# Kernel optimization log

Hardware: AMD Instinct MI355X
Metric: run time of the kernel (lower is better)

## Reference

```python
import jax, jax.numpy as jnp
import numpy as np

VOCAB = 50257
NSAMPLES = 1048576


def setup_inputs() -> dict:
    key = jax.random.key(0)
    k1, k2 = jax.random.split(key)
    # positive sampling weights (need not be normalized, as in WeightedRandomSampler)
    frequencies = jax.random.uniform(k1, (VOCAB,), dtype=jnp.float32) + 1e-3
    # pre-drawn uniforms, one per sample (replacement=True => iid draws)
    u = jax.random.uniform(k2, (NSAMPLES,), dtype=jnp.float32)
    return {"frequencies": frequencies, "u": u}


def reference(frequencies, u):
    # WeightedRandomSampler with replacement == multinomial sampling proportional
    # to frequencies. Implemented as inverse-CDF: normalize, cumsum, binary search.
    cdf = jnp.cumsum(frequencies)          # [V], unnormalized CDF
    total = cdf[-1]
    # scale uniforms into [0, total) instead of dividing the whole CDF (fewer ops)
    idx = jnp.searchsorted(cdf, u * total, side="right")  # [N] int indices
    idx = jnp.clip(idx, 0, frequencies.shape[0] - 1)
    # original returns a FloatTensor of the sampled indices
    return idx.astype(jnp.float32)
```

## Files before the change

kernel.cpp:

```cpp
#include <hip/hip_runtime.h>
#include <math.h>


#define GRP 4
#define TPB 512
#define SPT 4

__device__ __forceinline__ int physIdx(int i) { return i + (i >> 5); }

__global__ __launch_bounds__(256) void gsum_kernel(const float* __restrict__ freq,
                                                   int V, float* __restrict__ gsum) {
    const int g = blockIdx.x * 256 + threadIdx.x;
    const int G = (V + 3) >> 2;
    if (g >= G) return;
    const int base = g * 4;
    float s = 0.f;
    if (base + 3 < V) {
        const float4 v = *reinterpret_cast<const float4*>(freq + base);
        s = v.x + v.y + v.z + v.w;
    } else {
        for (int j = 0; j < 4; ++j)
            if (base + j < V) s += freq[base + j];
    }
    gsum[g] = s;
}

template <int PAD>
__global__ __launch_bounds__(TPB) void sample_kernel(const float* __restrict__ freq,
                                                     const float* __restrict__ u,
                                                     const float* __restrict__ gsum,
                                                     float* __restrict__ out,
                                                     int N, int V, int G) {
    constexpr int GPTM = PAD / TPB;
    __shared__ float sS[PAD + (PAD >> 5)];
    __shared__ float wsum[TPB / 64];
    const int t = threadIdx.x;
    const int lane = t & 63;
    const int w = t >> 6;
    const int GPT = (G + TPB - 1) / TPB;

    const int gid = blockIdx.x * TPB + t;
    const long long i0 = (long long)gid * SPT;
    float uk[SPT];
    const bool full = (i0 + SPT <= N);
    if (full) {
        const float4 A = *reinterpret_cast<const float4*>(u + i0);
        uk[0] = A.x; uk[1] = A.y; uk[2] = A.z; uk[3] = A.w;
    } else {
#pragma unroll
        for (int s = 0; s < SPT; ++s) uk[s] = (i0 + s < N) ? u[i0 + s] : 0.f;
    }

    const int G4 = G >> 2;
    const float4* gs4 = reinterpret_cast<const float4*>(gsum);
    float4* sS4 = reinterpret_cast<float4*>(sS);
    for (int i = t; i < G4; i += TPB) sS4[i] = gs4[i];
    for (int i = (G4 << 2) + t; i < G; i += TPB) sS[i] = gsum[i];
    __syncthreads();

    const int g0 = t * GPT;
    float ls[GPTM];
    float runv = 0.f;
#pragma unroll
    for (int k = 0; k < GPTM; ++k) {
        float s = 0.f;
        if (k < GPT) { const int g = g0 + k; if (g < G) s = sS[g]; }
        runv += s;
        ls[k] = runv;
    }
    float sc = runv;
#pragma unroll
    for (int off = 1; off <= 32; off <<= 1) {
        const float v = __shfl_up(sc, off);
        if (lane >= off) sc += v;
    }
    if (lane == 63) wsum[w] = sc;
    __syncthreads();
    float tbase = sc - runv;
    for (int k = 0; k < w; ++k) tbase += wsum[k];

#pragma unroll
    for (int k = 0; k < GPTM; ++k) {
        if (k < GPT) { const int g = g0 + k; if (g < G) sS[physIdx(g)] = tbase + ls[k]; }
    }
    for (int i = G + t; i < PAD; i += TPB) sS[physIdx(i)] = INFINITY;
    __syncthreads();

    if (i0 >= N) return;

    const float total = sS[physIdx(G - 1)];

    float ok[SPT];
#pragma unroll
    for (int s = 0; s < SPT; ++s) {
        const float key = uk[s] * total;

        int pos = -1;
#pragma unroll
        for (int step = PAD >> 1; step >= 1; step >>= 1) {
            const int j = pos + step;
            pos += (sS[physIdx(j)] <= key) ? step : 0;
        }
        int g = pos + 1;
        g = (g > G - 1) ? (G - 1) : g;
        const float base = (g > 0) ? sS[physIdx(g - 1)] : 0.f;
        const int eb = g << 2;

        float r = base;
        int cnt = 0;
        if (eb + 4 <= V) {
            const float4 f = *reinterpret_cast<const float4*>(freq + eb);
            r += f.x; cnt += (r <= key);
            r += f.y; cnt += (r <= key);
            r += f.z; cnt += (r <= key);
            r += f.w; cnt += (r <= key);
        } else {
            for (int j = 0; j < 4; ++j) {
                const int idx = eb + j;
                if (idx < V) { r += freq[idx]; cnt += (r <= key); }
            }
        }
        int ans = eb + cnt;
        ans = (ans > V - 1) ? (V - 1) : ans;
        ok[s] = (float)ans;
    }

    if (full) {
        *reinterpret_cast<float4*>(out + i0) = make_float4(ok[0], ok[1], ok[2], ok[3]);
    } else {
        for (int s = 0; s < SPT; ++s)
            if (i0 + s < N) out[i0 + s] = ok[s];
    }
}

extern "C" void kernel_launch(void* const* d_in, const int* in_sizes, int n_in,
                              void* d_out, int out_size, void* d_ws, size_t ws_size,
                              hipStream_t stream) {
    const float* freq = (const float*)d_in[0];
    const float* u    = (const float*)d_in[1];
    float* out        = (float*)d_out;
    const int V = in_sizes[0];
    const int N = in_sizes[1];
    const int G = (V + GRP - 1) / GRP;

    float* gsum = (float*)d_ws;

    hipLaunchKernelGGL(gsum_kernel, dim3((G + 255) / 256), dim3(256), 0, stream,
                       freq, V, gsum);

    const int NB = (N + TPB * SPT - 1) / (TPB * SPT);
    if (G < 2048) {
        hipLaunchKernelGGL(sample_kernel<2048>, dim3(NB), dim3(TPB), 0, stream,
                           freq, u, gsum, out, N, V, G);
    } else if (G < 4096) {
        hipLaunchKernelGGL(sample_kernel<4096>, dim3(NB), dim3(TPB), 0, stream,
                           freq, u, gsum, out, N, V, G);
    } else if (G < 8192) {
        hipLaunchKernelGGL(sample_kernel<8192>, dim3(NB), dim3(TPB), 0, stream,
                           freq, u, gsum, out, N, V, G);
    } else {
        hipLaunchKernelGGL(sample_kernel<16384>, dim3(NB), dim3(TPB), 0, stream,
                           freq, u, gsum, out, N, V, G);
    }
}
```

Baseline: 22.58 us.

## Replace shared-memory binary search with uniform-bucket lookup table plus linear walk

Each block now builds an 8192-entry lookup table in shared memory that maps a uniform bucket to the first group whose CDF covers it. Each sample starts from the table entry and walks linearly to the correct group, replacing the 14-step binary search. This cuts the dependent LDS loads per sample. In exchange every block does extra table-building work and adds a barrier, and the walk length depends on how the weights are distributed. The padded layout is dropped and a tighter 12800 template is added for the test vocabulary, lowering LDS use per block.

```diff
diff --git a/kernel.cpp b/kernel.cpp
--- a/kernel.cpp
+++ b/kernel.cpp
@@ -5,8 +5,7 @@
 #define GRP 4
 #define TPB 512
 #define SPT 4
-
-__device__ __forceinline__ int physIdx(int i) { return i + (i >> 5); }
+#define KLUT 8192
 
 __global__ __launch_bounds__(256) void gsum_kernel(const float* __restrict__ freq,
                                                    int V, float* __restrict__ gsum) {
@@ -25,14 +24,15 @@
     gsum[g] = s;
 }
 
-template <int PAD>
+template <int CAP>
 __global__ __launch_bounds__(TPB) void sample_kernel(const float* __restrict__ freq,
                                                      const float* __restrict__ u,
                                                      const float* __restrict__ gsum,
                                                      float* __restrict__ out,
                                                      int N, int V, int G) {
-    constexpr int GPTM = PAD / TPB;
-    __shared__ float sS[PAD + (PAD >> 5)];
+    constexpr int GPTM = (CAP + TPB - 1) / TPB;
+    __shared__ float cdfS[CAP];
+    __shared__ unsigned short lut[KLUT];
     __shared__ float wsum[TPB / 64];
     const int t = threadIdx.x;
     const int lane = t & 63;
@@ -51,11 +51,11 @@
         for (int s = 0; s < SPT; ++s) uk[s] = (i0 + s < N) ? u[i0 + s] : 0.f;
     }
 
-    const int G4 = G >> 2;
+    const int nf4 = G >> 2;
     const float4* gs4 = reinterpret_cast<const float4*>(gsum);
-    float4* sS4 = reinterpret_cast<float4*>(sS);
-    for (int i = t; i < G4; i += TPB) sS4[i] = gs4[i];
-    for (int i = (G4 << 2) + t; i < G; i += TPB) sS[i] = gsum[i];
+    float4* cd4 = reinterpret_cast<float4*>(cdfS);
+    for (int i = t; i < nf4; i += TPB) cd4[i] = gs4[i];
+    for (int i = (nf4 << 2) + t; i < G; i += TPB) cdfS[i] = gsum[i];
     __syncthreads();
 
     const int g0 = t * GPT;
@@ -64,7 +64,7 @@
 #pragma unroll
     for (int k = 0; k < GPTM; ++k) {
         float s = 0.f;
-        if (k < GPT) { const int g = g0 + k; if (g < G) s = sS[g]; }
+        if (k < GPT) { const int g = g0 + k; if (g < G) s = cdfS[g]; }
         runv += s;
         ls[k] = runv;
     }
@@ -81,29 +81,50 @@
 
 #pragma unroll
     for (int k = 0; k < GPTM; ++k) {
-        if (k < GPT) { const int g = g0 + k; if (g < G) sS[physIdx(g)] = tbase + ls[k]; }
+        if (k < GPT) { const int g = g0 + k; if (g < G) cdfS[g] = tbase + ls[k]; }
     }
-    for (int i = G + t; i < PAD; i += TPB) sS[physIdx(i)] = INFINITY;
+    for (int b = t; b < KLUT; b += TPB) {
+        int gg = (int)(((long long)b * G) >> 13);
+        lut[b] = (unsigned short)(gg > G - 1 ? G - 1 : gg);
+    }
+    __syncthreads();
+
+    const float total = cdfS[G - 1];
+    const float fK = (float)KLUT;
+    {
+        float cprev = tbase;
+#pragma unroll
+        for (int k = 0; k < GPTM; ++k) {
+            if (k < GPT) {
+                const int g = g0 + k;
+                if (g < G) {
+                    const float ccur = tbase + ls[k];
+                    int bl = (int)ceilf((cprev / total) * fK);
+                    int bh = (int)ceilf((ccur / total) * fK);
+                    bl = bl < 0 ? 0 : (bl > KLUT ? KLUT : bl);
+                    bh = bh < 0 ? 0 : (bh > KLUT ? KLUT : bh);
+                    for (int b = bl; b < bh; ++b) lut[b] = (unsigned short)g;
+                    cprev = ccur;
+                }
+            }
+        }
+    }
     __syncthreads();
 
     if (i0 >= N) return;
 
-    const float total = sS[physIdx(G - 1)];
-
     float ok[SPT];
 #pragma unroll
     for (int s = 0; s < SPT; ++s) {
-        const float key = uk[s] * total;
-
-        int pos = -1;
-#pragma unroll
-        for (int step = PAD >> 1; step >= 1; step >>= 1) {
-            const int j = pos + step;
-            pos += (sS[physIdx(j)] <= key) ? step : 0;
-        }
-        int g = pos + 1;
-        g = (g > G - 1) ? (G - 1) : g;
-        const float base = (g > 0) ? sS[physIdx(g - 1)] : 0.f;
+        const float uu = uk[s];
+        const float key = uu * total;
+        int b = (int)(uu * fK);
+        b = b < 0 ? 0 : (b > KLUT - 1 ? KLUT - 1 : b);
+        int g = lut[b];
+        if (g > G - 1) g = G - 1;
+        while (g < G - 1 && cdfS[g] <= key) ++g;
+        while (g > 0 && cdfS[g - 1] > key) --g;
+        const float base = (g > 0) ? cdfS[g - 1] : 0.f;
         const int eb = g << 2;
 
         float r = base;
@@ -149,14 +170,11 @@
                        freq, V, gsum);
 
     const int NB = (N + TPB * SPT - 1) / (TPB * SPT);
-    if (G < 2048) {
-        hipLaunchKernelGGL(sample_kernel<2048>, dim3(NB), dim3(TPB), 0, stream,
-                           freq, u, gsum, out, N, V, G);
-    } else if (G < 4096) {
+    if (G <= 4096) {
         hipLaunchKernelGGL(sample_kernel<4096>, dim3(NB), dim3(TPB), 0, stream,
                            freq, u, gsum, out, N, V, G);
-    } else if (G < 8192) {
-        hipLaunchKernelGGL(sample_kernel<8192>, dim3(NB), dim3(TPB), 0, stream,
+    } else if (G <= 12800) {
+        hipLaunchKernelGGL(sample_kernel<12800>, dim3(NB), dim3(TPB), 0, stream,
                            freq, u, gsum, out, N, V, G);
     } else {
         hipLaunchKernelGGL(sample_kernel<16384>, dim3(NB), dim3(TPB), 0, stream,
```

Result: slower. 28.51 us (+26.3%).
